# Kernel optimization log

Measured on AMD Instinct MI355X. Metric: run time of the kernel, lower is better.

Reference implementation:

```python
import jax, jax.numpy as jnp
import numpy as np

# Product fuzzy logic (embed-wise):
#   bin_xnor(a,b)    = a*b + (1-a)*(1-b)
#   implies(a,b)     = 1 - a*(1-b)
#   conjoin(x,dim)   = prod(x, dim)
#   bin_conjoin(a,b) = a*b
#   disjoin(x,dim)   = 1 - prod(1-x, dim)

B, IN_F, HID_F, OUT_F, E = 128, 256, 512, 128, 8

def setup_inputs() -> dict:
    key = jax.random.key(0)
    k0, k1, k2, k3 = jax.random.split(key, 4)
    return {
        "input": jax.random.uniform(k0, (B, IN_F, E), dtype=jnp.float32),
        "conj_weights": jax.random.uniform(k1, (IN_F, HID_F, E), dtype=jnp.float32),
        "conj_signs": jax.random.uniform(k2, (IN_F, HID_F, E), dtype=jnp.float32),
        "disj_weights": jax.random.uniform(k3, (HID_F, OUT_F, E), dtype=jnp.float32),
    }

def reference(input, conj_weights, conj_signs, disj_weights):
    # --- EmbedSignedConjunction ---
    x = input[:, :, None, :]                      # [B, in, 1, E]
    xnor = x * conj_signs + (1.0 - x) * (1.0 - conj_signs)   # [B, in, hid, E]
    impl = 1.0 - conj_weights * (1.0 - xnor)      # implies(w, xnor)
    h = jnp.prod(impl, axis=1)                    # conjoin over in -> [B, hid, E]

    # --- EmbedUnsignedDisjunction ---
    hh = h[:, :, None, :]                         # [B, hid, 1, E]
    conj = disj_weights * hh                      # bin_conjoin -> [B, hid, out, E]
    out = 1.0 - jnp.prod(1.0 - conj, axis=1)      # disjoin over hid -> [B, out, E]
    return out
```

## Files before the change

### kernel.cpp

```cpp
#include <hip/hip_runtime.h>


#define LD4(p) (*(const float4*)(p))

static __device__ __forceinline__ float4 f4mul(float4 a, float4 b) {
    return make_float4(a.x*b.x, a.y*b.y, a.z*b.z, a.w*b.w);
}
static __device__ __forceinline__ float4 f4fma(float4 a, float4 b, float4 c) {
    return make_float4(fmaf(a.x,b.x,c.x), fmaf(a.y,b.y,c.y),
                       fmaf(a.z,b.z,c.z), fmaf(a.w,b.w,c.w));
}
static __device__ __forceinline__ float4 f4nfma1(float4 d, float4 h) {
    return make_float4(fmaf(-d.x,h.x,1.0f), fmaf(-d.y,h.y,1.0f),
                       fmaf(-d.z,h.z,1.0f), fmaf(-d.w,h.w,1.0f));
}

__global__ __launch_bounds__(256, 4) void k_stage1(
    const float* __restrict__ in,
    const float* __restrict__ cw,
    const float* __restrict__ cs,
    float* __restrict__ P1)
{
    __shared__ float lds[4096];
    const int t    = threadIdx.x;
    const int lane = t & 63;
    const int kc   = t >> 6;
    const int eh   = lane & 1;
    const int hl   = lane >> 1;
    const int hg   = blockIdx.x & 15;
    const int bg   = (blockIdx.x >> 4) & 15;
    const int ks   = blockIdx.x >> 8;
    const int b0   = bg * 8;
    const int h    = hg * 32 + hl;
    const int e0   = eh * 4;

    {
        float4* xs4 = (float4*)lds;
        #pragma unroll
        for (int k = 0; k < 2; ++k) {
            const int f4  = t + k * 256;
            const int b   = f4 >> 6;
            const int col = f4 & 63;
            xs4[f4] = LD4(in + (b0 + b) * 2048 + ks * 256 + col * 4);
        }
    }
    __syncthreads();

    const int i0 = ks * 32 + kc * 8;
    const float* pw = cw + i0 * 4096 + h * 8 + e0;
    const float* ps = cs + i0 * 4096 + h * 8 + e0;
    const float* xbase = lds + kc * 64 + e0;

    float4 acc[8];
    #pragma unroll
    for (int b = 0; b < 8; ++b) acc[b] = make_float4(1.f, 1.f, 1.f, 1.f);

    #pragma unroll
    for (int ii = 0; ii < 8; ++ii) {
        const float4 wv = LD4(pw);
        const float4 sv = LD4(ps);
        pw += 4096; ps += 4096;
        const float4 p  = f4mul(wv, sv);
        const float4 A  = make_float4(1.f - p.x, 1.f - p.y, 1.f - p.z, 1.f - p.w);
        const float4 Bv = make_float4(fmaf(2.f, p.x, -wv.x), fmaf(2.f, p.y, -wv.y),
                                      fmaf(2.f, p.z, -wv.z), fmaf(2.f, p.w, -wv.w));
        #pragma unroll
        for (int b = 0; b < 8; ++b) {
            const float4 xv = LD4(xbase + b * 256 + ii * 8);
            acc[b] = f4mul(acc[b], f4fma(xv, Bv, A));
        }
    }

    __syncthreads();
    #pragma unroll
    for (int phase = 0; phase < 2; ++phase) {
        if (phase) __syncthreads();
        #pragma unroll
        for (int j = 0; j < 4; ++j)
            *(float4*)&lds[kc * 1024 + j * 256 + hl * 8 + e0] = acc[phase * 4 + j];
        __syncthreads();
        {
            const int o4 = t * 4;
            float4 m = LD4(&lds[o4]);
            #pragma unroll
            for (int c = 1; c < 4; ++c) m = f4mul(m, LD4(&lds[c * 1024 + o4]));
            const int j   = o4 >> 8;
            const int hl2 = (o4 >> 3) & 31;
            const int eq  = o4 & 7;
            *(float4*)(P1 + ks * 524288 + (hg * 32 + hl2) * 1024
                          + (b0 + phase * 4 + j) * 8 + eq) = m;
        }
    }
}

__global__ __launch_bounds__(256, 4) void k_stage2(
    const float* __restrict__ dw,
    const float* __restrict__ P1,
    float* __restrict__ P2)
{
    __shared__ float lds[4096];
    const int t    = threadIdx.x;
    const int lane = t & 63;
    const int kc   = t >> 6;
    const int eh   = lane & 1;
    const int ol   = lane >> 1;
    const int og   = blockIdx.x & 3;
    const int bg   = (blockIdx.x >> 2) & 15;
    const int ks   = blockIdx.x >> 6;
    const int b0   = bg * 8;
    const int o    = og * 32 + ol;
    const int e0   = eh * 4;
    const int h0   = ks * 32;

    {
        float4* ht4 = (float4*)lds;
        #pragma unroll
        for (int k = 0; k < 2; ++k) {
            const int f4  = t + k * 256;
            const int hl  = f4 >> 4;
            const int rem = f4 & 15;
            const float* q = P1 + (h0 + hl) * 1024 + b0 * 8 + rem * 4;
            float4 m = LD4(q);
            #pragma unroll
            for (int c = 1; c < 8; ++c) m = f4mul(m, LD4(q + c * 524288));
            ht4[f4] = m;
        }
    }
    __syncthreads();

    const float* pd = dw + (h0 + kc * 8) * 1024 + o * 8 + e0;
    const float* hbase = lds + kc * 512 + e0;

    float4 acc[8];
    #pragma unroll
    for (int b = 0; b < 8; ++b) acc[b] = make_float4(1.f, 1.f, 1.f, 1.f);

    #pragma unroll
    for (int ii = 0; ii < 8; ++ii) {
        const float4 dv = LD4(pd);
        pd += 1024;
        #pragma unroll
        for (int b = 0; b < 8; ++b) {
            const float4 hv = LD4(hbase + ii * 64 + b * 8);
            acc[b] = f4mul(acc[b], f4nfma1(dv, hv));
        }
    }

    __syncthreads();
    #pragma unroll
    for (int phase = 0; phase < 2; ++phase) {
        if (phase) __syncthreads();
        #pragma unroll
        for (int j = 0; j < 4; ++j)
            *(float4*)&lds[kc * 1024 + j * 256 + ol * 8 + e0] = acc[phase * 4 + j];
        __syncthreads();
        {
            const int o4 = t * 4;
            float4 m = LD4(&lds[o4]);
            #pragma unroll
            for (int c = 1; c < 4; ++c) m = f4mul(m, LD4(&lds[c * 1024 + o4]));
            const int j   = o4 >> 8;
            const int ol2 = (o4 >> 3) & 31;
            const int eq  = o4 & 7;
            *(float4*)(P2 + ks * 131072 + (b0 + phase * 4 + j) * 1024
                          + (og * 32 + ol2) * 8 + eq) = m;
        }
    }
}

__global__ __launch_bounds__(256, 4) void k_comb2(
    const float* __restrict__ P2,
    float* __restrict__ out)
{
    const int idx4 = blockIdx.x * 256 + threadIdx.x;
    float4 m = LD4(P2 + idx4 * 4);
    #pragma unroll
    for (int c = 1; c < 16; ++c)
        m = f4mul(m, LD4(P2 + c * 131072 + idx4 * 4));
    const float4 r = make_float4(1.f - m.x, 1.f - m.y, 1.f - m.z, 1.f - m.w);
    *(float4*)(out + idx4 * 4) = r;
}

extern "C" void kernel_launch(void* const* d_in, const int* in_sizes, int n_in,
                              void* d_out, int out_size, void* d_ws, size_t ws_size,
                              hipStream_t stream)
{
    const float* in = (const float*)d_in[0];
    const float* cw = (const float*)d_in[1];
    const float* cs = (const float*)d_in[2];
    const float* dw = (const float*)d_in[3];
    float* outp = (float*)d_out;
    float* P1   = (float*)d_ws;
    float* P2   = (float*)d_ws + 4194304;

    k_stage1<<<2048, 256, 0, stream>>>(in, cw, cs, P1);
    k_stage2<<<1024, 256, 0, stream>>>(dw, P1, P2);
    k_comb2<<<128, 256, 0, stream>>>(P2, outp);
}
```

Measured before the change: 96.20 us.

## Retile stage2 so each block covers all outputs for two batch rows

Each stage2 block previously handled 32 outputs for 8 batch rows. It now handles all 128 outputs for 2 batch rows, with 64 batch groups per k-split. This cuts the redundant 8-way reduction of P1 partials: every P1 element is now combined once per block instead of four times across output groups. In exchange, the disjunction weights are reused across only 2 batches instead of 8, so weight reads from cache increase fourfold.

```diff
diff --git a/kernel.cpp b/kernel.cpp
--- a/kernel.cpp
+++ b/kernel.cpp
@@ -104,46 +104,50 @@
     const int kc   = t >> 6;
     const int eh   = lane & 1;
     const int ol   = lane >> 1;
-    const int og   = blockIdx.x & 3;
-    const int bg   = (blockIdx.x >> 2) & 15;
+    const int bg   = blockIdx.x & 63;
     const int ks   = blockIdx.x >> 6;
-    const int b0   = bg * 8;
-    const int o    = og * 32 + ol;
+    const int b0   = bg * 2;
     const int e0   = eh * 4;
     const int h0   = ks * 32;
 
-    {
-        float4* ht4 = (float4*)lds;
-        #pragma unroll
-        for (int k = 0; k < 2; ++k) {
-            const int f4  = t + k * 256;
-            const int hl  = f4 >> 4;
-            const int rem = f4 & 15;
-            const float* q = P1 + (h0 + hl) * 1024 + b0 * 8 + rem * 4;
-            float4 m = LD4(q);
-            #pragma unroll
-            for (int c = 1; c < 8; ++c) m = f4mul(m, LD4(q + c * 524288));
-            ht4[f4] = m;
-        }
-    }
-    __syncthreads();
-
-    const float* pd = dw + (h0 + kc * 8) * 1024 + o * 8 + e0;
-    const float* hbase = lds + kc * 512 + e0;
-
-    float4 acc[8];
-    #pragma unroll
-    for (int b = 0; b < 8; ++b) acc[b] = make_float4(1.f, 1.f, 1.f, 1.f);
+    if (t < 128) {
+        const int hl = t >> 2;
+        const int b  = (t >> 1) & 1;
+        const int eq = (t & 1) * 4;
+        const float* q = P1 + (h0 + hl) * 1024 + (b0 + b) * 8 + eq;
+        float4 m = LD4(q);
+        #pragma unroll
+        for (int c = 1; c < 8; ++c) m = f4mul(m, LD4(q + c * 524288));
+        ((float4*)lds)[t] = m;
+    }
+    __syncthreads();
+
+    const float* pd = dw + (h0 + kc * 8) * 1024 + ol * 8 + e0;
+    const float* hbase = lds + kc * 128 + e0;
+
+    float4 acc[4][2];
+    #pragma unroll
+    for (int q = 0; q < 4; ++q)
+        #pragma unroll
+        for (int b = 0; b < 2; ++b) acc[q][b] = make_float4(1.f, 1.f, 1.f, 1.f);
 
     #pragma unroll
     for (int ii = 0; ii < 8; ++ii) {
-        const float4 dv = LD4(pd);
+        const float4 dv0 = LD4(pd);
+        const float4 dv1 = LD4(pd + 256);
+        const float4 dv2 = LD4(pd + 512);
+        const float4 dv3 = LD4(pd + 768);
         pd += 1024;
-        #pragma unroll
-        for (int b = 0; b < 8; ++b) {
-            const float4 hv = LD4(hbase + ii * 64 + b * 8);
-            acc[b] = f4mul(acc[b], f4nfma1(dv, hv));
-        }
+        const float4 hv0 = LD4(hbase + ii * 16);
+        const float4 hv1 = LD4(hbase + ii * 16 + 8);
+        acc[0][0] = f4mul(acc[0][0], f4nfma1(dv0, hv0));
+        acc[1][0] = f4mul(acc[1][0], f4nfma1(dv1, hv0));
+        acc[2][0] = f4mul(acc[2][0], f4nfma1(dv2, hv0));
+        acc[3][0] = f4mul(acc[3][0], f4nfma1(dv3, hv0));
+        acc[0][1] = f4mul(acc[0][1], f4nfma1(dv0, hv1));
+        acc[1][1] = f4mul(acc[1][1], f4nfma1(dv1, hv1));
+        acc[2][1] = f4mul(acc[2][1], f4nfma1(dv2, hv1));
+        acc[3][1] = f4mul(acc[3][1], f4nfma1(dv3, hv1));
     }
 
     __syncthreads();
@@ -151,19 +155,19 @@
     for (int phase = 0; phase < 2; ++phase) {
         if (phase) __syncthreads();
         #pragma unroll
-        for (int j = 0; j < 4; ++j)
-            *(float4*)&lds[kc * 1024 + j * 256 + ol * 8 + e0] = acc[phase * 4 + j];
+        for (int q = 0; q < 4; ++q)
+            *(float4*)&lds[kc * 1024 + q * 256 + ol * 8 + e0] = acc[q][phase];
         __syncthreads();
         {
             const int o4 = t * 4;
             float4 m = LD4(&lds[o4]);
             #pragma unroll
             for (int c = 1; c < 4; ++c) m = f4mul(m, LD4(&lds[c * 1024 + o4]));
-            const int j   = o4 >> 8;
+            const int q   = o4 >> 8;
             const int ol2 = (o4 >> 3) & 31;
             const int eq  = o4 & 7;
-            *(float4*)(P2 + ks * 131072 + (b0 + phase * 4 + j) * 1024
-                          + (og * 32 + ol2) * 8 + eq) = m;
+            *(float4*)(P2 + ks * 131072 + (b0 + phase) * 1024
+                          + (q * 32 + ol2) * 8 + eq) = m;
         }
     }
 }
```

Measured after the change: 128.8 us. 1.34x slower.
